# Kernel optimization log

Hardware: AMD Instinct MI355X
Metric: run time of the kernel (lower is better)

Reference implementation:

```python
import jax, jax.numpy as jnp
import numpy as np

VOCAB = 32000
HIDDEN = 2048
NLAYERS = 6
BATCH = 512


def setup_inputs() -> dict:
    key = jax.random.key(0)
    k1, k2, k3, k4 = jax.random.split(key, 4)
    state = jax.random.normal(k1, (BATCH, HIDDEN), dtype=jnp.float32)
    token = jax.random.randint(k2, (BATCH,), 0, VOCAB, dtype=jnp.int32)
    ih = jax.random.normal(k3, (NLAYERS, VOCAB, HIDDEN), dtype=jnp.float32) * 0.02
    hh = jax.random.normal(k4, (NLAYERS, HIDDEN, HIDDEN), dtype=jnp.float32) * 0.02
    return {"state": state, "token": token, "ih": ih, "hh": hh}


def reference(state, token, ih, hh):
    # Per layer: state = tanh(state + (state @ hh[i]) * ih[i][token])
    n_layers = ih.shape[0]
    for i in range(n_layers):
        gate = ih[i][token]                  # [B, H] embedding gather
        state = jnp.tanh(state + jnp.matmul(state, hh[i]) * gate)
    return state
```

## Files before the change

kernel.cpp:

```cpp
#include <hip/hip_runtime.h>
#include <hip/hip_bf16.h>
#include <cstdint>
#include <cstddef>

#define VOCAB 32000
#define HIDDEN 2048
#define NLAYERS 6
#define BATCH 512

#define BM 128
#define BN 64
#define BK 64
#define SPLITK 4
#define KC (HIDDEN / SPLITK)
#define NT (KC / BK)

typedef __attribute__((ext_vector_type(8))) short bf16x8;
typedef __attribute__((ext_vector_type(4))) float f32x4;

__device__ __forceinline__ unsigned short f2bf(float f) {
  unsigned u = __builtin_bit_cast(unsigned, f);
  u += 0x7fffu + ((u >> 16) & 1u);
  return (unsigned short)(u >> 16);
}

__device__ __forceinline__ float bf2f(unsigned short h) {
  return __builtin_bit_cast(float, (unsigned)h << 16);
}

__device__ __forceinline__ float tanh_fast(float x) {
  x = fminf(15.f, fmaxf(-15.f, x));
  float e = __expf(2.f * x);
  return (e - 1.f) / (e + 1.f);
}

__device__ __forceinline__ void gload_lds16(const void* g, void* l) {
  __builtin_amdgcn_global_load_lds(
      (const __attribute__((address_space(1))) void*)g,
      (__attribute__((address_space(3))) void*)l, 16, 0, 0);
}

__global__ __launch_bounds__(256) void k_prep(const float* __restrict__ hh,
                                              unsigned short* __restrict__ bt,
                                              const float* __restrict__ state,
                                              unsigned short* __restrict__ stb) {
  const int l = blockIdx.z;
  const int t = threadIdx.x;
  if (l == NLAYERS) {
    const int bid = blockIdx.y * 32 + blockIdx.x;
    const int i = (bid * 256 + t) * 4;
    float4 v = *(const float4*)(state + i);
    union { unsigned short h[4]; uint2 u; } o;
    o.h[0] = f2bf(v.x); o.h[1] = f2bf(v.y); o.h[2] = f2bf(v.z); o.h[3] = f2bf(v.w);
    *(uint2*)(stb + i) = o.u;
    return;
  }
  __shared__ unsigned short tile[64][72];
  const int n0 = blockIdx.x * 64;
  const int k0 = blockIdx.y * 64;
  const float* src = hh + ((size_t)l * HIDDEN + k0) * HIDDEN + n0;
  const int cr = t >> 4;
  const int cc = (t & 15) * 4;
#pragma unroll
  for (int p = 0; p < 4; ++p) {
    const int r = p * 16 + cr;
    float4 v = *(const float4*)(src + (size_t)r * HIDDEN + cc);
    tile[r][cc + 0] = f2bf(v.x);
    tile[r][cc + 1] = f2bf(v.y);
    tile[r][cc + 2] = f2bf(v.z);
    tile[r][cc + 3] = f2bf(v.w);
  }
  __syncthreads();
  const int nl = t >> 2;
  const int kk = (t & 3) * 16;
  unsigned short tmp[16] __attribute__((aligned(16)));
#pragma unroll
  for (int j = 0; j < 16; ++j) tmp[j] = tile[kk + j][nl];
  unsigned short* dst = bt + ((size_t)l * HIDDEN + n0 + nl) * HIDDEN + k0 + kk;
  *(uint4*)(dst) = *(const uint4*)(tmp);
  *(uint4*)(dst + 8) = *(const uint4*)(tmp + 8);
}

__global__ __launch_bounds__(256, 2) void k_gemm(const unsigned short* __restrict__ A,
                                                 const unsigned short* __restrict__ Bt,
                                                 unsigned short* __restrict__ part) {
  __shared__ __attribute__((aligned(16))) unsigned short As[2][BM][BK];
  __shared__ __attribute__((aligned(16))) unsigned short Bs[2][BN][BK];

  const int n0 = blockIdx.x * BN;
  const int m0 = blockIdx.y * BM;
  const int kz = blockIdx.z;
  const int kbase = kz * KC;
  const int t = threadIdx.x;
  const int lane = t & 63;
  const int wid = t >> 6;
  const int wm = (wid >> 1) * 64;
  const int wn = (wid & 1) * 32;

  f32x4 zero = {0.f, 0.f, 0.f, 0.f};
  f32x4 acc[4][2];
#pragma unroll
  for (int i = 0; i < 4; ++i) { acc[i][0] = zero; acc[i][1] = zero; }

  const int r0 = t >> 3;
  const int sc = ((t & 7) ^ (r0 & 7)) * 8;
  const unsigned short* gA = A + (size_t)(m0 + r0) * HIDDEN + kbase + sc;
  const unsigned short* gB = Bt + (size_t)(n0 + r0) * HIDDEN + kbase + sc;
  char* lA = (char*)&As[0][0][0] + wid * 1024;
  char* lB = (char*)&Bs[0][0][0] + wid * 1024;

#define STAGE(buf, kt)                                                     \
  do {                                                                     \
    const int ko = (kt)*BK;                                                \
    gload_lds16(gA + ko, lA + (buf)*16384);                                \
    gload_lds16(gA + 32 * HIDDEN + ko, lA + (buf)*16384 + 4096);           \
    gload_lds16(gA + 64 * HIDDEN + ko, lA + (buf)*16384 + 8192);           \
    gload_lds16(gA + 96 * HIDDEN + ko, lA + (buf)*16384 + 12288);          \
    gload_lds16(gB + ko, lB + (buf)*8192);                                 \
    gload_lds16(gB + 32 * HIDDEN + ko, lB + (buf)*8192 + 4096);            \
  } while (0)

  const int ra = wm + (lane & 15);
  const int rb = wn + (lane & 15);
  const int q = lane >> 4;

#define COMPUTE(buf)                                                                      \
  do {                                                                                    \
    _Pragma("unroll") for (int ks = 0; ks < 2; ++ks) {                                    \
      const int cnk = ks * 4 + q;                                                         \
      bf16x8 b0 = *(const bf16x8*)&Bs[buf][rb][(cnk ^ (rb & 7)) * 8];                     \
      bf16x8 b1 = *(const bf16x8*)&Bs[buf][rb + 16][(cnk ^ ((rb + 16) & 7)) * 8];         \
      _Pragma("unroll") for (int fm = 0; fm < 4; ++fm) {                                  \
        const int r = ra + fm * 16;                                                       \
        bf16x8 a = *(const bf16x8*)&As[buf][r][(cnk ^ (r & 7)) * 8];                      \
        acc[fm][0] = __builtin_amdgcn_mfma_f32_16x16x32_bf16(a, b0, acc[fm][0], 0, 0, 0); \
        acc[fm][1] = __builtin_amdgcn_mfma_f32_16x16x32_bf16(a, b1, acc[fm][1], 0, 0, 0); \
      }                                                                                   \
    }                                                                                     \
  } while (0)

  STAGE(0, 0);
  __syncthreads();
  for (int kt = 0; kt < NT; ++kt) {
    const int buf = kt & 1;
    if (kt + 1 < NT) STAGE(buf ^ 1, kt + 1);
    COMPUTE(buf);
    __syncthreads();
  }

  unsigned short* p = part + (size_t)kz * ((size_t)BATCH * HIDDEN);
  const int orow = m0 + wm + (q << 2);
  const int ocol = n0 + wn + (lane & 15);
#pragma unroll
  for (int fm = 0; fm < 4; ++fm)
#pragma unroll
    for (int fn = 0; fn < 2; ++fn)
#pragma unroll
      for (int j = 0; j < 4; ++j)
        p[(size_t)(orow + fm * 16 + j) * HIDDEN + ocol + fn * 16] = f2bf(acc[fm][fn][j]);
}

__global__ __launch_bounds__(256) void k_reduce(const unsigned short* __restrict__ part,
                                                const float* __restrict__ prev,
                                                const float* __restrict__ ihl,
                                                const int* __restrict__ token,
                                                float* __restrict__ outf,
                                                unsigned short* __restrict__ outb) {
  const int idx = (blockIdx.x * 256 + threadIdx.x) * 4;
  const int m = idx >> 11;
  const int n = idx & 2047;
  const size_t MN = (size_t)BATCH * HIDDEN;
  float s[4] = {0.f, 0.f, 0.f, 0.f};
#pragma unroll
  for (int kz = 0; kz < SPLITK; ++kz) {
    union { uint2 u; unsigned short h[4]; } v;
    v.u = *(const uint2*)(part + kz * MN + idx);
#pragma unroll
    for (int j = 0; j < 4; ++j) s[j] += bf2f(v.h[j]);
  }
  float4 pv = *(const float4*)(prev + idx);
  const int tok = token[m];
  float4 g = *(const float4*)(ihl + (size_t)tok * HIDDEN + n);
  float4 r;
  r.x = tanh_fast(pv.x + s[0] * g.x);
  r.y = tanh_fast(pv.y + s[1] * g.y);
  r.z = tanh_fast(pv.z + s[2] * g.z);
  r.w = tanh_fast(pv.w + s[3] * g.w);
  *(float4*)(outf + idx) = r;
  if (outb) {
    union { unsigned short h[4]; uint2 u; } o;
    o.h[0] = f2bf(r.x); o.h[1] = f2bf(r.y); o.h[2] = f2bf(r.z); o.h[3] = f2bf(r.w);
    *(uint2*)(outb + idx) = o.u;
  }
}

extern "C" void kernel_launch(void* const* d_in, const int* in_sizes, int n_in,
                              void* d_out, int out_size, void* d_ws, size_t ws_size,
                              hipStream_t stream) {
  const float* state = (const float*)d_in[0];
  const int* token = (const int*)d_in[1];
  const float* ih = (const float*)d_in[2];
  const float* hh = (const float*)d_in[3];
  float* out = (float*)d_out;

  char* ws = (char*)d_ws;
  unsigned short* bt = (unsigned short*)ws;
  size_t off = (size_t)NLAYERS * HIDDEN * HIDDEN * 2;
  unsigned short* stb = (unsigned short*)(ws + off);
  off += (size_t)BATCH * HIDDEN * 2;
  float* sf = (float*)(ws + off);
  off += (size_t)BATCH * HIDDEN * 4;
  unsigned short* part = (unsigned short*)(ws + off);

  k_prep<<<dim3(HIDDEN / 64, HIDDEN / 64, NLAYERS + 1), 256, 0, stream>>>(hh, bt, state, stb);

  for (int l = 0; l < NLAYERS; ++l) {
    const bool last = (l == NLAYERS - 1);
    k_gemm<<<dim3(HIDDEN / BN, BATCH / BM, SPLITK), 256, 0, stream>>>(
        stb, bt + (size_t)l * HIDDEN * HIDDEN, part);
    k_reduce<<<dim3((BATCH * HIDDEN) / 1024), 256, 0, stream>>>(
        part, l == 0 ? state : sf, ih + (size_t)l * VOCAB * HIDDEN, token,
        last ? out : sf, last ? nullptr : stb);
  }
}
```

Baseline: 126.9 us.

## Switch GEMM to 32x32x16 MFMA with 128x128 tiles and split-K 8

Replaces the 16x16x32 MFMA inner loop with 32x32x16 MFMA, doubles the N tile to 128, and raises split-K from 4 to 8 so the grid keeps enough blocks. Each wave now computes a 64x64 sub-tile with four 32x32 accumulators, which gives more reuse per LDS fragment load and fewer MFMA issues. The cost is more partial buffers for the reduce kernel to read and write, higher register pressure, and a scattered epilogue store pattern. The reduce kernel and partial buffer sizing must also handle SPLITK=8, which depends on the unseen code using the macro.

```diff
diff --git a/kernel.cpp b/kernel.cpp
--- a/kernel.cpp
+++ b/kernel.cpp
@@ -9,14 +9,14 @@
 #define BATCH 512
 
 #define BM 128
-#define BN 64
+#define BN 128
 #define BK 64
-#define SPLITK 4
+#define SPLITK 8
 #define KC (HIDDEN / SPLITK)
 #define NT (KC / BK)
 
 typedef __attribute__((ext_vector_type(8))) short bf16x8;
-typedef __attribute__((ext_vector_type(4))) float f32x4;
+typedef __attribute__((ext_vector_type(16))) float f32x16;
 
 __device__ __forceinline__ unsigned short f2bf(float f) {
   unsigned u = __builtin_bit_cast(unsigned, f);
@@ -95,12 +95,9 @@
   const int lane = t & 63;
   const int wid = t >> 6;
   const int wm = (wid >> 1) * 64;
-  const int wn = (wid & 1) * 32;
-
-  f32x4 zero = {0.f, 0.f, 0.f, 0.f};
-  f32x4 acc[4][2];
-#pragma unroll
-  for (int i = 0; i < 4; ++i) { acc[i][0] = zero; acc[i][1] = zero; }
+  const int wn = (wid & 1) * 64;
+
+  f32x16 acc00 = {0}, acc01 = {0}, acc10 = {0}, acc11 = {0};
 
   const int r0 = t >> 3;
   const int sc = ((t & 7) ^ (r0 & 7)) * 8;
@@ -109,34 +106,37 @@
   char* lA = (char*)&As[0][0][0] + wid * 1024;
   char* lB = (char*)&Bs[0][0][0] + wid * 1024;
 
-#define STAGE(buf, kt)                                                     \
-  do {                                                                     \
-    const int ko = (kt)*BK;                                                \
-    gload_lds16(gA + ko, lA + (buf)*16384);                                \
-    gload_lds16(gA + 32 * HIDDEN + ko, lA + (buf)*16384 + 4096);           \
-    gload_lds16(gA + 64 * HIDDEN + ko, lA + (buf)*16384 + 8192);           \
-    gload_lds16(gA + 96 * HIDDEN + ko, lA + (buf)*16384 + 12288);          \
-    gload_lds16(gB + ko, lB + (buf)*8192);                                 \
-    gload_lds16(gB + 32 * HIDDEN + ko, lB + (buf)*8192 + 4096);            \
+#define STAGE(buf, kt)                                            \
+  do {                                                            \
+    const int ko = (kt)*BK;                                       \
+    gload_lds16(gA + ko, lA + (buf)*16384);                       \
+    gload_lds16(gA + 32 * HIDDEN + ko, lA + (buf)*16384 + 4096);  \
+    gload_lds16(gA + 64 * HIDDEN + ko, lA + (buf)*16384 + 8192);  \
+    gload_lds16(gA + 96 * HIDDEN + ko, lA + (buf)*16384 + 12288); \
+    gload_lds16(gB + ko, lB + (buf)*16384);                       \
+    gload_lds16(gB + 32 * HIDDEN + ko, lB + (buf)*16384 + 4096);  \
+    gload_lds16(gB + 64 * HIDDEN + ko, lB + (buf)*16384 + 8192);  \
+    gload_lds16(gB + 96 * HIDDEN + ko, lB + (buf)*16384 + 12288); \
   } while (0)
 
-  const int ra = wm + (lane & 15);
-  const int rb = wn + (lane & 15);
-  const int q = lane >> 4;
-
-#define COMPUTE(buf)                                                                      \
-  do {                                                                                    \
-    _Pragma("unroll") for (int ks = 0; ks < 2; ++ks) {                                    \
-      const int cnk = ks * 4 + q;                                                         \
-      bf16x8 b0 = *(const bf16x8*)&Bs[buf][rb][(cnk ^ (rb & 7)) * 8];                     \
-      bf16x8 b1 = *(const bf16x8*)&Bs[buf][rb + 16][(cnk ^ ((rb + 16) & 7)) * 8];         \
-      _Pragma("unroll") for (int fm = 0; fm < 4; ++fm) {                                  \
-        const int r = ra + fm * 16;                                                       \
-        bf16x8 a = *(const bf16x8*)&As[buf][r][(cnk ^ (r & 7)) * 8];                      \
-        acc[fm][0] = __builtin_amdgcn_mfma_f32_16x16x32_bf16(a, b0, acc[fm][0], 0, 0, 0); \
-        acc[fm][1] = __builtin_amdgcn_mfma_f32_16x16x32_bf16(a, b1, acc[fm][1], 0, 0, 0); \
-      }                                                                                   \
-    }                                                                                     \
+  const int rowA0 = wm + (lane & 31);
+  const int rowB0 = wn + (lane & 31);
+  const int hk = lane >> 5;
+  const int swz = rowA0 & 7;
+
+#define COMPUTE(buf)                                                                   \
+  do {                                                                                 \
+    _Pragma("unroll") for (int ks = 0; ks < 4; ++ks) {                                 \
+      const int cnk = ((ks * 2 + hk) ^ swz) * 8;                                       \
+      bf16x8 a0 = *(const bf16x8*)&As[buf][rowA0][cnk];                                \
+      bf16x8 a1 = *(const bf16x8*)&As[buf][rowA0 + 32][cnk];                           \
+      bf16x8 b0 = *(const bf16x8*)&Bs[buf][rowB0][cnk];                                \
+      bf16x8 b1 = *(const bf16x8*)&Bs[buf][rowB0 + 32][cnk];                           \
+      acc00 = __builtin_amdgcn_mfma_f32_32x32x16_bf16(a0, b0, acc00, 0, 0, 0);         \
+      acc01 = __builtin_amdgcn_mfma_f32_32x32x16_bf16(a0, b1, acc01, 0, 0, 0);         \
+      acc10 = __builtin_amdgcn_mfma_f32_32x32x16_bf16(a1, b0, acc10, 0, 0, 0);         \
+      acc11 = __builtin_amdgcn_mfma_f32_32x32x16_bf16(a1, b1, acc11, 0, 0, 0);         \
+    }                                                                                  \
   } while (0)
 
   STAGE(0, 0);
@@ -149,15 +149,19 @@
   }
 
   unsigned short* p = part + (size_t)kz * ((size_t)BATCH * HIDDEN);
-  const int orow = m0 + wm + (q << 2);
-  const int ocol = n0 + wn + (lane & 15);
-#pragma unroll
-  for (int fm = 0; fm < 4; ++fm)
-#pragma unroll
-    for (int fn = 0; fn < 2; ++fn)
-#pragma unroll
-      for (int j = 0; j < 4; ++j)
-        p[(size_t)(orow + fm * 16 + j) * HIDDEN + ocol + fn * 16] = f2bf(acc[fm][fn][j]);
+  const int colb = n0 + wn + (lane & 31);
+  const int rowb = m0 + wm + 4 * hk;
+#define STORE_ACC(accv, fm, fn)                                                   \
+  do {                                                                            \
+    _Pragma("unroll") for (int r = 0; r < 16; ++r) {                              \
+      const int rl = (r & 3) + 8 * (r >> 2);                                      \
+      p[(size_t)(rowb + (fm)*32 + rl) * HIDDEN + colb + (fn)*32] = f2bf(accv[r]); \
+    }                                                                             \
+  } while (0)
+  STORE_ACC(acc00, 0, 0);
+  STORE_ACC(acc01, 0, 1);
+  STORE_ACC(acc10, 1, 0);
+  STORE_ACC(acc11, 1, 1);
 }
 
 __global__ __launch_bounds__(256) void k_reduce(const unsigned short* __restrict__ part,
```

New measurement: 131.2 us. 3.4% more time.
